# Kernel optimization log

Hardware: AMD Instinct MI355X
Metric: run time of the kernel (lower is better)

Reference implementation:

```python
import jax, jax.numpy as jnp
import numpy as np

DIM = 1024
N_HEADS = 16
HEAD_DIM = DIM // N_HEADS
B, T = 2, 2048
ROPE_THETA = 32.0
EPS = 1e-6


def precompute_freqs_1d(dim, seq_len, theta):
    freqs = theta ** (-jnp.arange(0, dim, 2, dtype=jnp.float32) / dim)  # [dim/2]
    t = jnp.arange(seq_len, dtype=jnp.float32)
    ang = t[:, None] * freqs[None, :]  # [T, dim/2]
    return jnp.cos(ang), jnp.sin(ang)


def setup_inputs() -> dict:
    key = jax.random.key(0)
    k1, k2, k3, k4, k5 = jax.random.split(key, 5)
    x = jax.random.normal(k1, (B, T, DIM), dtype=jnp.float32)
    w_qkv = jax.random.normal(k2, (3 * DIM, DIM), dtype=jnp.float32) * (DIM ** -0.5)
    w_proj = jax.random.normal(k3, (DIM, DIM), dtype=jnp.float32) * (DIM ** -0.5)
    q_norm_w = 1.0 + 0.1 * jax.random.normal(k4, (HEAD_DIM,), dtype=jnp.float32)
    k_norm_w = 1.0 + 0.1 * jax.random.normal(k5, (HEAD_DIM,), dtype=jnp.float32)
    return {"x": x, "w_qkv": w_qkv, "w_proj": w_proj,
            "q_norm_w": q_norm_w, "k_norm_w": k_norm_w}


def _rms_norm(t, w):
    # t: [B,H,T,hd]; normalize over last dim
    var = jnp.mean(t * t, axis=-1, keepdims=True)
    return t * jax.lax.rsqrt(var + EPS) * w


def _rope(q, k, cos, sin):
    # cos/sin: [T, hd/2] -> [1,1,T,hd/2]
    cos = cos[None, None]
    sin = sin[None, None]
    q1, q2 = jnp.split(q, 2, axis=-1)
    k1, k2 = jnp.split(k, 2, axis=-1)
    q_out = jnp.concatenate([q1 * cos - q2 * sin, q2 * cos + q1 * sin], axis=-1)
    k_out = jnp.concatenate([k1 * cos - k2 * sin, k2 * cos + k1 * sin], axis=-1)
    return q_out, k_out


def reference(x, w_qkv, w_proj, q_norm_w, k_norm_w):
    Bc, Tc, C = x.shape
    scale = HEAD_DIM ** -0.5
    qkv = x @ w_qkv.T  # [B,T,3*C]
    qkv = qkv.reshape(Bc, Tc, 3, N_HEADS, HEAD_DIM).transpose(2, 0, 3, 1, 4)
    q, k, v = qkv[0], qkv[1], qkv[2]  # each [B,H,T,hd]
    q = _rms_norm(q, q_norm_w)
    k = _rms_norm(k, k_norm_w)
    cos, sin = precompute_freqs_1d(HEAD_DIM, Tc, ROPE_THETA)
    q, k = _rope(q, k, cos, sin)
    attn = jnp.einsum('bhqd,bhkd->bhqk', q, k) * scale
    causal = jnp.triu(jnp.ones((Tc, Tc), dtype=bool), k=1)
    attn = jnp.where(causal, -jnp.inf, attn)
    attn = jax.nn.softmax(attn, axis=-1)
    out = jnp.einsum('bhqk,bhkd->bhqd', attn, v)  # [B,H,T,hd]
    out = out.transpose(0, 2, 1, 3).reshape(Bc, Tc, C)
    return out @ w_proj.T
```

## Files before the change

kernel.cpp:

```cpp
#include <hip/hip_runtime.h>
#include <hip/hip_bf16.h>

#define DIM   1024
#define NH    16
#define HD    64
#define BB    2
#define TT    2048
#define BT    (BB*TT)
#define BHN   (BB*NH)

typedef __attribute__((ext_vector_type(8))) __bf16 bf16x8;
typedef __attribute__((ext_vector_type(4))) float  f32x4;

__device__ __forceinline__ unsigned short f2bf(float f) {
    unsigned int u = __float_as_uint(f);
    u = (u + 0x7fffu + ((u >> 16) & 1u)) >> 16;
    return (unsigned short)u;
}

__device__ __forceinline__ void gload_lds16(const unsigned short* g, unsigned short* l) {
    __builtin_amdgcn_global_load_lds(
        (const __attribute__((address_space(1))) unsigned int*)g,
        (__attribute__((address_space(3))) unsigned int*)l, 16, 0, 0);
}

__global__ __launch_bounds__(256) void cvt_bf16(const float* __restrict__ in,
                                                unsigned short* __restrict__ out, int n) {
    int i = blockIdx.x * 256 + threadIdx.x;
    int base = i * 8;
    if (base >= n) return;
    float4 a = *reinterpret_cast<const float4*>(in + base);
    float4 b = *reinterpret_cast<const float4*>(in + base + 4);
    uint4 o;
    o.x = (unsigned)f2bf(a.x) | ((unsigned)f2bf(a.y) << 16);
    o.y = (unsigned)f2bf(a.z) | ((unsigned)f2bf(a.w) << 16);
    o.z = (unsigned)f2bf(b.x) | ((unsigned)f2bf(b.y) << 16);
    o.w = (unsigned)f2bf(b.z) | ((unsigned)f2bf(b.w) << 16);
    *reinterpret_cast<uint4*>(out + base) = o;
}

__global__ __launch_bounds__(256) void build_rope(float* __restrict__ cosT,
                                                  float* __restrict__ sinT) {
    int i = blockIdx.x * 256 + threadIdx.x;
    if (i >= TT * 32) return;
    int t = i >> 5, j = i & 31;
    float freq = exp2f(-5.0f * (float)j * (1.0f / 32.0f));
    float ang  = (float)t * freq;
    cosT[i] = cosf(ang);
    sinT[i] = sinf(ang);
}

__global__ __launch_bounds__(256) void gemm_bt(const unsigned short* __restrict__ A,
                                               const unsigned short* __restrict__ Bt,
                                               float* __restrict__ C,
                                               int M, int N, int K) {
    __shared__ alignas(16) unsigned short sA[128 * 64];
    __shared__ alignas(16) unsigned short sB[128 * 64];
    const int t    = threadIdx.x;
    const int nb   = N >> 7;
    const int m0   = (blockIdx.x / nb) << 7;
    const int n0   = (blockIdx.x % nb) << 7;
    const int w    = t >> 6, lane = t & 63;
    const int wr   = w >> 1, wc = w & 1;
    const int lrow = lane & 15, lk = lane >> 4;
    const int r_   = t >> 3;
    const int c_   = t & 7;
    const int pg   = c_ ^ (r_ & 7);

    f32x4 acc[4][4] = {};

    for (int kt = 0; kt < K; kt += 64) {
        __syncthreads();
#pragma unroll
        for (int i = 0; i < 4; i++) {
            gload_lds16(A  + (size_t)(m0 + i * 32 + r_) * K + kt + pg * 8, sA + i * 2048 + w * 512);
            gload_lds16(Bt + (size_t)(n0 + i * 32 + r_) * K + kt + pg * 8, sB + i * 2048 + w * 512);
        }
        __syncthreads();
#pragma unroll
        for (int ks = 0; ks < 2; ks++) {
            bf16x8 af[4], bfr[4];
#pragma unroll
            for (int mi = 0; mi < 4; mi++) {
                int rowa = wr * 64 + mi * 16 + lrow;
                int ga   = (ks * 4 + lk) ^ (rowa & 7);
                af[mi]   = *reinterpret_cast<const bf16x8*>(&sA[rowa * 64 + ga * 8]);
                int rowb = wc * 64 + mi * 16 + lrow;
                int gb   = (ks * 4 + lk) ^ (rowb & 7);
                bfr[mi]  = *reinterpret_cast<const bf16x8*>(&sB[rowb * 64 + gb * 8]);
            }
#pragma unroll
            for (int mi = 0; mi < 4; mi++)
#pragma unroll
                for (int ni = 0; ni < 4; ni++)
                    acc[mi][ni] = __builtin_amdgcn_mfma_f32_16x16x32_bf16(af[mi], bfr[ni], acc[mi][ni], 0, 0, 0);
        }
    }
#pragma unroll
    for (int mi = 0; mi < 4; mi++)
#pragma unroll
        for (int ni = 0; ni < 4; ni++) {
            int row = m0 + wr * 64 + mi * 16 + lk * 4;
            int col = n0 + wc * 64 + ni * 16 + lrow;
#pragma unroll
            for (int i = 0; i < 4; i++)
                C[(size_t)(row + i) * N + col] = acc[mi][ni][i];
        }
}

__global__ __launch_bounds__(256) void norm_rope(const float* __restrict__ qkv,
                                                 const float* __restrict__ cosT,
                                                 const float* __restrict__ sinT,
                                                 const float* __restrict__ qw,
                                                 const float* __restrict__ kw,
                                                 unsigned short* __restrict__ Qo,
                                                 unsigned short* __restrict__ Ko,
                                                 unsigned short* __restrict__ Vo) {
    int wv = threadIdx.x >> 6, lane = threadIdx.x & 63;
    int rid = blockIdx.x * 4 + wv;
    int sel = rid >> 16;
    int rem = rid & 65535;
    int h   = rem & 15;
    int bt  = rem >> 4;
    int tp  = bt & (TT - 1);
    int b   = bt >> 11;
    float v = qkv[(size_t)bt * 3072 + sel * 1024 + h * 64 + lane];
    unsigned short* dst = (sel == 0) ? Qo : ((sel == 1) ? Ko : Vo);
    size_t didx = ((size_t)(b * NH + h) * TT + tp) * 64 + lane;
    float outv;
    if (sel < 2) {
        float ss = v * v;
#pragma unroll
        for (int m = 32; m; m >>= 1) ss += __shfl_xor(ss, m);
        float r = rsqrtf(ss * (1.0f / 64.0f) + 1e-6f);
        const float* wgt = sel ? kw : qw;
        float nv = v * r * wgt[lane];
        float other = __shfl_xor(nv, 32);
        int j = lane & 31;
        float c = cosT[tp * 32 + j], s = sinT[tp * 32 + j];
        outv = (lane < 32) ? (nv * c - other * s) : (nv * c + other * s);
        if (sel == 0) outv *= 0.125f;
    } else {
        outv = v;
    }
    dst[didx] = f2bf(outv);
}

__global__ __launch_bounds__(256) void transpose_v(const unsigned short* __restrict__ Vb,
                                                   unsigned short* __restrict__ Vt) {
    __shared__ unsigned short s[64 * 68];
    const int t0 = blockIdx.x * 64, bh = blockIdx.y;
    const unsigned short* src = Vb + (size_t)bh * TT * 64;
    const int r = threadIdx.x >> 2, g4 = threadIdx.x & 3;
#pragma unroll
    for (int p = 0; p < 2; p++) {
        int g = g4 + p * 4;
        *reinterpret_cast<uint4*>(&s[r * 68 + g * 8]) =
            *reinterpret_cast<const uint4*>(src + (size_t)(t0 + r) * 64 + g * 8);
    }
    __syncthreads();
#pragma unroll
    for (int p = 0; p < 2; p++) {
        int tt = (g4 + p * 4) * 8;
        unsigned short tmp[8];
#pragma unroll
        for (int j = 0; j < 8; j++) tmp[j] = s[(tt + j) * 68 + r];
        *reinterpret_cast<uint4*>(Vt + ((size_t)bh * 64 + r) * TT + t0 + tt) =
            *reinterpret_cast<uint4*>(tmp);
    }
}

__global__ __launch_bounds__(256) void attn_fwd(const unsigned short* __restrict__ Qm,
                                                const unsigned short* __restrict__ Km,
                                                const unsigned short* __restrict__ Vt,
                                                unsigned short* __restrict__ Om) {
    __shared__ alignas(16) unsigned short sQ[64 * 68];
    __shared__ alignas(16) unsigned short sK[64 * 68];
    __shared__ alignas(16) unsigned short sVT[64 * 68];
    __shared__ alignas(16) unsigned short sP[4][16 * 68];
    const int bh = blockIdx.y;
    const int qt = (blockIdx.x + blockIdx.y) & 31;
    const int b = bh >> 4, h = bh & 15;
    const unsigned short* Qp = Qm + (size_t)bh * TT * 64;
    const unsigned short* Kp = Km + (size_t)bh * TT * 64;
    const unsigned short* Vp = Vt + (size_t)bh * 64 * TT;
    const int t = threadIdx.x, wv = t >> 6, lane = t & 63;
    const int lrow = lane & 15, lk = lane >> 4;
    const int r_ = t >> 3, c_ = t & 7;
    const int d_ = t >> 2, g_ = t & 3;

#pragma unroll
    for (int i = 0; i < 2; i++) {
        int r = i * 32 + r_;
        *reinterpret_cast<uint4*>(&sQ[r * 68 + c_ * 8]) =
            *reinterpret_cast<const uint4*>(Qp + (size_t)(qt * 64 + r) * 64 + c_ * 8);
    }
    __syncthreads();
    bf16x8 aq0 = *reinterpret_cast<const bf16x8*>(&sQ[(wv * 16 + lrow) * 68 + lk * 8]);
    bf16x8 aq1 = *reinterpret_cast<const bf16x8*>(&sQ[(wv * 16 + lrow) * 68 + 32 + lk * 8]);

    f32x4 o[4] = {};
    float mrun[4], lrun[4];
#pragma unroll
    for (int i = 0; i < 4; i++) { mrun[i] = -__builtin_inff(); lrun[i] = 0.0f; }

    for (int kt = 0; kt <= qt; kt++) {
        __syncthreads();
#pragma unroll
        for (int i = 0; i < 2; i++) {
            int r = i * 32 + r_;
            *reinterpret_cast<uint4*>(&sK[r * 68 + c_ * 8]) =
                *reinterpret_cast<const uint4*>(Kp + (size_t)(kt * 64 + r) * 64 + c_ * 8);
        }
#pragma unroll
        for (int p = 0; p < 2; p++) {
            int g = g_ + p * 4;
            *reinterpret_cast<uint4*>(&sVT[d_ * 68 + g * 8]) =
                *reinterpret_cast<const uint4*>(Vp + (size_t)d_ * TT + kt * 64 + g * 8);
        }
        __syncthreads();

        f32x4 s[4];
#pragma unroll
        for (int nt = 0; nt < 4; nt++) {
            f32x4 z = {0.f, 0.f, 0.f, 0.f};
            z = __builtin_amdgcn_mfma_f32_16x16x32_bf16(
                aq0, *reinterpret_cast<const bf16x8*>(&sK[(nt * 16 + lrow) * 68 + lk * 8]), z, 0, 0, 0);
            z = __builtin_amdgcn_mfma_f32_16x16x32_bf16(
                aq1, *reinterpret_cast<const bf16x8*>(&sK[(nt * 16 + lrow) * 68 + 32 + lk * 8]), z, 0, 0, 0);
            s[nt] = z;
        }
        if (kt == qt) {
#pragma unroll
            for (int nt = 0; nt < 4; nt++)
#pragma unroll
                for (int i = 0; i < 4; i++)
                    if (nt * 16 + lrow > wv * 16 + lk * 4 + i) s[nt][i] = -__builtin_inff();
        }

        float tm[4], ts[4], fsc[4];
#pragma unroll
        for (int i = 0; i < 4; i++) {
            float a = fmaxf(fmaxf(s[0][i], s[1][i]), fmaxf(s[2][i], s[3][i]));
#pragma unroll
            for (int msk = 8; msk; msk >>= 1) a = fmaxf(a, __shfl_xor(a, msk));
            tm[i] = a;
        }
#pragma unroll
        for (int i = 0; i < 4; i++) {
            float mn = fmaxf(mrun[i], tm[i]);
            fsc[i] = __expf(mrun[i] - mn);
            mrun[i] = mn;
            ts[i] = 0.f;
        }
#pragma unroll
        for (int nt = 0; nt < 4; nt++)
#pragma unroll
            for (int i = 0; i < 4; i++) {
                float p = __expf(s[nt][i] - mrun[i]);
                s[nt][i] = p;
                ts[i] += p;
            }
#pragma unroll
        for (int i = 0; i < 4; i++) {
            float a = ts[i];
#pragma unroll
            for (int msk = 8; msk; msk >>= 1) a += __shfl_xor(a, msk);
            lrun[i] = lrun[i] * fsc[i] + a;
        }
#pragma unroll
        for (int dt = 0; dt < 4; dt++)
#pragma unroll
            for (int i = 0; i < 4; i++) o[dt][i] *= fsc[i];

        unsigned short* myP = &sP[wv][0];
#pragma unroll
        for (int nt = 0; nt < 4; nt++)
#pragma unroll
            for (int i = 0; i < 4; i++)
                myP[(lk * 4 + i) * 68 + nt * 16 + lrow] = f2bf(s[nt][i]);
        bf16x8 pa0 = *reinterpret_cast<const bf16x8*>(&myP[lrow * 68 + lk * 8]);
        bf16x8 pa1 = *reinterpret_cast<const bf16x8*>(&myP[lrow * 68 + 32 + lk * 8]);
#pragma unroll
        for (int dt = 0; dt < 4; dt++) {
            o[dt] = __builtin_amdgcn_mfma_f32_16x16x32_bf16(
                pa0, *reinterpret_cast<const bf16x8*>(&sVT[(dt * 16 + lrow) * 68 + lk * 8]), o[dt], 0, 0, 0);
            o[dt] = __builtin_amdgcn_mfma_f32_16x16x32_bf16(
                pa1, *reinterpret_cast<const bf16x8*>(&sVT[(dt * 16 + lrow) * 68 + 32 + lk * 8]), o[dt], 0, 0, 0);
        }
    }

#pragma unroll
    for (int i = 0; i < 4; i++) lrun[i] = 1.0f / lrun[i];
    int qrow = qt * 64 + wv * 16 + lk * 4;
#pragma unroll
    for (int dt = 0; dt < 4; dt++)
#pragma unroll
        for (int i = 0; i < 4; i++) {
            size_t idx = ((size_t)(b * TT + qrow + i)) * 1024 + h * 64 + dt * 16 + lrow;
            Om[idx] = f2bf(o[dt][i] * lrun[i]);
        }
}

extern "C" void kernel_launch(void* const* d_in, const int* in_sizes, int n_in,
                              void* d_out, int out_size, void* d_ws, size_t ws_size,
                              hipStream_t stream) {
    const float* x      = (const float*)d_in[0];
    const float* w_qkv  = (const float*)d_in[1];
    const float* w_proj = (const float*)d_in[2];
    const float* qw     = (const float*)d_in[3];
    const float* kw     = (const float*)d_in[4];
    float* out = (float*)d_out;
    char* ws = (char*)d_ws;

    unsigned short* xb     = (unsigned short*)(ws + 0);
    unsigned short* wqkvb  = (unsigned short*)(ws + 8388608);
    unsigned short* wprojb = (unsigned short*)(ws + 14680064);
    float*          qkvf   = (float*)(ws + 16777216);
    unsigned short* Vtb    = (unsigned short*)(ws + 16777216);
    unsigned short* Qb     = (unsigned short*)(ws + 67108864);
    unsigned short* Kb     = (unsigned short*)(ws + 75497472);
    unsigned short* Vb     = (unsigned short*)(ws + 83886080);
    float*          cosT   = (float*)(ws + 92274688);
    float*          sinT   = (float*)(ws + 92536832);
    unsigned short* attnb  = xb;

    cvt_bf16<<<2048, 256, 0, stream>>>(x, xb, BT * DIM);
    cvt_bf16<<<1536, 256, 0, stream>>>(w_qkv, wqkvb, 3 * DIM * DIM);
    cvt_bf16<<<512, 256, 0, stream>>>(w_proj, wprojb, DIM * DIM);
    build_rope<<<256, 256, 0, stream>>>(cosT, sinT);
    gemm_bt<<<(BT / 128) * (3 * DIM / 128), 256, 0, stream>>>(xb, wqkvb, qkvf, BT, 3 * DIM, DIM);
    norm_rope<<<3 * BT * NH / 4, 256, 0, stream>>>(qkvf, cosT, sinT, qw, kw, Qb, Kb, Vb);
    transpose_v<<<dim3(TT / 64, BHN), 256, 0, stream>>>(Vb, Vtb);
    attn_fwd<<<dim3(TT / 64, BHN), 256, 0, stream>>>(Qb, Kb, Vtb, attnb);
    gemm_bt<<<(BT / 128) * (DIM / 128), 256, 0, stream>>>(attnb, wprojb, out, BT, DIM, DIM);
    (void)in_sizes; (void)n_in; (void)out_size; (void)ws_size;
}
```

Measured before the change: 281.2 us.

## Prefetch K/V tiles into registers and use lazy rescaling with exp2 softmax

The attention loop now loads the next K and V tile into registers while the current tile is computed, then stores them to shared memory after the PV MMA, so global latency overlaps with compute. Softmax switches to exp2 by folding log2(e) into the Q scale. The running max is only rescaled when some row's new max exceeds the old one by more than 8. The row sum is kept per lane and reduced across lanes once at the end. This removes per-tile shuffles and exps at the cost of higher register pressure and possibly larger unnormalized values.

```diff
diff --git a/kernel.cpp b/kernel.cpp
--- a/kernel.cpp
+++ b/kernel.cpp
@@ -139,7 +139,7 @@
         int j = lane & 31;
         float c = cosT[tp * 32 + j], s = sinT[tp * 32 + j];
         outv = (lane < 32) ? (nv * c - other * s) : (nv * c + other * s);
-        if (sel == 0) outv *= 0.125f;
+        if (sel == 0) outv *= 0.125f * 1.4426950408889634f;
     } else {
         outv = v;
     }
@@ -195,30 +195,39 @@
         *reinterpret_cast<uint4*>(&sQ[r * 68 + c_ * 8]) =
             *reinterpret_cast<const uint4*>(Qp + (size_t)(qt * 64 + r) * 64 + c_ * 8);
     }
+    uint4 kreg[2], vreg[2];
+#pragma unroll
+    for (int i = 0; i < 2; i++)
+        kreg[i] = *reinterpret_cast<const uint4*>(Kp + (size_t)(i * 32 + r_) * 64 + c_ * 8);
+#pragma unroll
+    for (int p = 0; p < 2; p++)
+        vreg[p] = *reinterpret_cast<const uint4*>(Vp + (size_t)d_ * TT + (g_ + p * 4) * 8);
+#pragma unroll
+    for (int i = 0; i < 2; i++)
+        *reinterpret_cast<uint4*>(&sK[(i * 32 + r_) * 68 + c_ * 8]) = kreg[i];
+#pragma unroll
+    for (int p = 0; p < 2; p++)
+        *reinterpret_cast<uint4*>(&sVT[d_ * 68 + (g_ + p * 4) * 8]) = vreg[p];
     __syncthreads();
+
     bf16x8 aq0 = *reinterpret_cast<const bf16x8*>(&sQ[(wv * 16 + lrow) * 68 + lk * 8]);
     bf16x8 aq1 = *reinterpret_cast<const bf16x8*>(&sQ[(wv * 16 + lrow) * 68 + 32 + lk * 8]);
 
     f32x4 o[4] = {};
-    float mrun[4], lrun[4];
-#pragma unroll
-    for (int i = 0; i < 4; i++) { mrun[i] = -__builtin_inff(); lrun[i] = 0.0f; }
+    float mrun[4], lsum[4];
+#pragma unroll
+    for (int i = 0; i < 4; i++) { mrun[i] = -__builtin_inff(); lsum[i] = 0.0f; }
 
     for (int kt = 0; kt <= qt; kt++) {
-        __syncthreads();
-#pragma unroll
-        for (int i = 0; i < 2; i++) {
-            int r = i * 32 + r_;
-            *reinterpret_cast<uint4*>(&sK[r * 68 + c_ * 8]) =
-                *reinterpret_cast<const uint4*>(Kp + (size_t)(kt * 64 + r) * 64 + c_ * 8);
-        }
-#pragma unroll
-        for (int p = 0; p < 2; p++) {
-            int g = g_ + p * 4;
-            *reinterpret_cast<uint4*>(&sVT[d_ * 68 + g * 8]) =
-                *reinterpret_cast<const uint4*>(Vp + (size_t)d_ * TT + kt * 64 + g * 8);
-        }
-        __syncthreads();
+        const bool more = (kt < qt);
+        if (more) {
+#pragma unroll
+            for (int i = 0; i < 2; i++)
+                kreg[i] = *reinterpret_cast<const uint4*>(Kp + (size_t)((kt + 1) * 64 + i * 32 + r_) * 64 + c_ * 8);
+#pragma unroll
+            for (int p = 0; p < 2; p++)
+                vreg[p] = *reinterpret_cast<const uint4*>(Vp + (size_t)d_ * TT + (kt + 1) * 64 + (g_ + p * 4) * 8);
+        }
 
         f32x4 s[4];
 #pragma unroll
@@ -238,40 +247,36 @@
                     if (nt * 16 + lrow > wv * 16 + lk * 4 + i) s[nt][i] = -__builtin_inff();
         }
 
-        float tm[4], ts[4], fsc[4];
-#pragma unroll
-        for (int i = 0; i < 4; i++) {
-            float a = fmaxf(fmaxf(s[0][i], s[1][i]), fmaxf(s[2][i], s[3][i]));
-#pragma unroll
-            for (int msk = 8; msk; msk >>= 1) a = fmaxf(a, __shfl_xor(a, msk));
-            tm[i] = a;
-        }
-#pragma unroll
-        for (int i = 0; i < 4; i++) {
-            float mn = fmaxf(mrun[i], tm[i]);
-            fsc[i] = __expf(mrun[i] - mn);
-            mrun[i] = mn;
-            ts[i] = 0.f;
+        float pm[4];
+#pragma unroll
+        for (int i = 0; i < 4; i++)
+            pm[i] = fmaxf(fmaxf(s[0][i], s[1][i]), fmaxf(s[2][i], s[3][i]));
+        bool skip = __all(pm[0] <= mrun[0] + 8.0f && pm[1] <= mrun[1] + 8.0f &&
+                          pm[2] <= mrun[2] + 8.0f && pm[3] <= mrun[3] + 8.0f);
+        if (!skip) {
+#pragma unroll
+            for (int i = 0; i < 4; i++) {
+                float a = pm[i];
+#pragma unroll
+                for (int msk = 8; msk; msk >>= 1) a = fmaxf(a, __shfl_xor(a, msk));
+                float mn = fmaxf(mrun[i], a);
+                float fsc = exp2f(mrun[i] - mn);
+                mrun[i] = mn;
+                lsum[i] *= fsc;
+#pragma unroll
+                for (int dt = 0; dt < 4; dt++) o[dt][i] *= fsc;
+            }
         }
 #pragma unroll
         for (int nt = 0; nt < 4; nt++)
 #pragma unroll
             for (int i = 0; i < 4; i++) {
-                float p = __expf(s[nt][i] - mrun[i]);
+                float p = exp2f(s[nt][i] - mrun[i]);
                 s[nt][i] = p;
-                ts[i] += p;
             }
 #pragma unroll
-        for (int i = 0; i < 4; i++) {
-            float a = ts[i];
-#pragma unroll
-            for (int msk = 8; msk; msk >>= 1) a += __shfl_xor(a, msk);
-            lrun[i] = lrun[i] * fsc[i] + a;
-        }
-#pragma unroll
-        for (int dt = 0; dt < 4; dt++)
-#pragma unroll
-            for (int i = 0; i < 4; i++) o[dt][i] *= fsc[i];
+        for (int i = 0; i < 4; i++)
+            lsum[i] += (s[0][i] + s[1][i]) + (s[2][i] + s[3][i]);
 
         unsigned short* myP = &sP[wv][0];
 #pragma unroll
@@ -288,17 +293,34 @@
             o[dt] = __builtin_amdgcn_mfma_f32_16x16x32_bf16(
                 pa1, *reinterpret_cast<const bf16x8*>(&sVT[(dt * 16 + lrow) * 68 + 32 + lk * 8]), o[dt], 0, 0, 0);
         }
-    }
-
-#pragma unroll
-    for (int i = 0; i < 4; i++) lrun[i] = 1.0f / lrun[i];
+
+        __syncthreads();
+        if (more) {
+#pragma unroll
+            for (int i = 0; i < 2; i++)
+                *reinterpret_cast<uint4*>(&sK[(i * 32 + r_) * 68 + c_ * 8]) = kreg[i];
+#pragma unroll
+            for (int p = 0; p < 2; p++)
+                *reinterpret_cast<uint4*>(&sVT[d_ * 68 + (g_ + p * 4) * 8]) = vreg[p];
+            __syncthreads();
+        }
+    }
+
+    float inv[4];
+#pragma unroll
+    for (int i = 0; i < 4; i++) {
+        float a = lsum[i];
+#pragma unroll
+        for (int msk = 8; msk; msk >>= 1) a += __shfl_xor(a, msk);
+        inv[i] = 1.0f / a;
+    }
     int qrow = qt * 64 + wv * 16 + lk * 4;
 #pragma unroll
     for (int dt = 0; dt < 4; dt++)
 #pragma unroll
         for (int i = 0; i < 4; i++) {
             size_t idx = ((size_t)(b * TT + qrow + i)) * 1024 + h * 64 + dt * 16 + lrow;
-            Om[idx] = f2bf(o[dt][i] * lrun[i]);
+            Om[idx] = f2bf(o[dt][i] * inv[i]);
         }
 }
 
```

New measurement: 304.3 us. 8.2% more time.
